# Kernel optimization log

Measured on AMD Instinct MI355X. Metric: run time of the kernel, lower is better.

The kernel has to match this reference:

```python
import jax, jax.numpy as jnp
import numpy as np

N_HEAD = 16
N_KV_HEAD = 4
D_HEAD = 128
RMS_EPS = 1.1920929e-07  # torch default eps for fp32 rms_norm


def _rms_norm(x):
    return x * jax.lax.rsqrt(jnp.mean(x * x, axis=-1, keepdims=True) + RMS_EPS)


def _rotary_tables(n_pos, dim):
    # dim = d_head; freq table has dim//2 entries (half of them zero)
    angular_freq = (1.0 / 1024.0) ** jnp.linspace(0.0, 1.0, dim // 4, dtype=jnp.float32)
    angular_freq = jnp.concatenate([angular_freq, jnp.zeros(dim // 4, jnp.float32)])
    theta = jnp.arange(n_pos, dtype=jnp.float32)[:, None] * angular_freq[None, :]
    return jnp.cos(theta), jnp.sin(theta)


def _apply_rotary(x):
    # x: (B, H, T, D). Faithful to source: cos/sin indexed by x.shape[-3] (= H),
    # broadcast over the time axis.
    n = x.shape[-3]
    cos, sin = _rotary_tables(n, x.shape[-1])
    cos = cos[None, :, None, :]
    sin = sin[None, :, None, :]
    xf = x.astype(jnp.float32)
    x1, x2 = jnp.split(xf, 2, axis=-1)
    y1 = x1 * cos + x2 * sin
    y2 = -x1 * sin + x2 * cos
    return jnp.concatenate([y1, y2], axis=-1).astype(x.dtype)


def setup_inputs() -> dict:
    key = jax.random.key(0)
    k1, k2, k3, k4 = jax.random.split(key, 4)
    B, T, C = 2, 2048, 2048
    return {
        "x": jax.random.normal(k1, (B, T, C), jnp.float32),
        "Wq": jax.random.normal(k2, (C, C), jnp.float32) * 0.02,
        "Wkv": jax.random.normal(k3, (2 * N_KV_HEAD * D_HEAD, C), jnp.float32) * 0.02,
        "Wproj": jax.random.normal(k4, (C, C), jnp.float32) * 0.02,
        "tok_masks": jnp.ones((B, T), jnp.int32),
    }


def reference(x, Wq, Wkv, Wproj, tok_masks):
    B, T, C = x.shape
    nh, nkv, dh = N_HEAD, N_KV_HEAD, D_HEAD

    q = (x @ Wq.T).reshape(B, T, nh, dh).transpose(0, 2, 1, 3)          # (B,nh,T,dh)
    kv = x @ Wkv.T                                                       # (B,T,2*nkv*dh)
    k, v = jnp.split(kv, 2, axis=2)
    k = k.reshape(B, T, nkv, dh).transpose(0, 2, 1, 3)                   # (B,nkv,T,dh)
    v = v.reshape(B, T, nkv, dh).transpose(0, 2, 1, 3)

    q, k = _rms_norm(q), _rms_norm(k)
    q, k = _apply_rotary(q), _apply_rotary(k)

    # GQA: repeat kv heads to match query heads
    rep = nh // nkv
    k = jnp.repeat(k, rep, axis=1)
    v = jnp.repeat(v, rep, axis=1)

    scale = 1.0 / jnp.sqrt(jnp.float32(dh))
    scores = jnp.einsum("bhqd,bhkd->bhqk", q, k) * scale                 # (B,nh,T,T)
    causal = jnp.tril(jnp.ones((T, T), bool))
    scores = jnp.where(causal[None, None], scores, -jnp.inf)
    attn = jax.nn.softmax(scores, axis=-1)
    y = jnp.einsum("bhqk,bhkd->bhqd", attn, v)                           # (B,nh,T,dh)
    y = y.transpose(0, 2, 1, 3).reshape(B, T, C)
    y = y @ Wproj.T
    return (y, jnp.float32(0.0))
```

## Files before the change

kernel.cpp:

```cpp
#include <hip/hip_runtime.h>
#include <hip/hip_bf16.h>

#define T_SEQ 2048
#define BATCH 2
#define CDIM  2048
#define NH    16
#define NKV   4
#define DH    128

typedef __attribute__((ext_vector_type(8))) short bfrag;
typedef __attribute__((ext_vector_type(4))) float ffrag;
typedef __hip_bfloat16 bf16;

#if defined(__has_builtin)
#if __has_builtin(__builtin_amdgcn_global_load_lds)
#define USE_GLL 1
#endif
#endif
#ifndef USE_GLL
#define USE_GLL 0
#endif

__device__ __forceinline__ void stage16(const bf16* __restrict__ g, bf16* lds_base, int lane) {
#if USE_GLL
    __builtin_amdgcn_global_load_lds((const __attribute__((address_space(1))) void*)g,
                                     (__attribute__((address_space(3))) void*)lds_base, 16, 0, 0);
#else
    *(bfrag*)(lds_base + lane * 8) = *(const bfrag*)g;
#endif
}

struct bf16x4 { bf16 a, b, c, d; };
#define N4_X   (BATCH * T_SEQ * CDIM / 4)
#define N4_WQ  (CDIM * CDIM / 4)
#define N4_WKV (2 * NKV * DH * CDIM / 4)
#define N4_WP  (CDIM * CDIM / 4)
__global__ __launch_bounds__(256) void cast_all(
    const float* __restrict__ x, const float* __restrict__ wq,
    const float* __restrict__ wkv, const float* __restrict__ wp,
    bf16* __restrict__ xb, bf16* __restrict__ wqb, bf16* __restrict__ wkvb, bf16* __restrict__ wpb)
{
    int j = blockIdx.x * 256 + threadIdx.x;
    const float* s; bf16* d;
    if (j < N4_X) { s = x; d = xb; }
    else {
        j -= N4_X;
        if (j < N4_WQ) { s = wq; d = wqb; }
        else {
            j -= N4_WQ;
            if (j < N4_WKV) { s = wkv; d = wkvb; }
            else { j -= N4_WKV; if (j >= N4_WP) return; s = wp; d = wpb; }
        }
    }
    float4 f = ((const float4*)s)[j];
    bf16x4 o{__float2bfloat16(f.x), __float2bfloat16(f.y),
             __float2bfloat16(f.z), __float2bfloat16(f.w)};
    ((bf16x4*)d)[j] = o;
}

template<int MODE>
__device__ __forceinline__ void gemm_body(
    const bf16* __restrict__ A, const bf16* __restrict__ W, int m0, int n0,
    bf16* __restrict__ out0, bf16* __restrict__ out1, float* __restrict__ outf)
{
    __shared__ __align__(16) bf16 sA[128 * 32];
    __shared__ __align__(16) bf16 sB[128 * 32];
    const int lane = threadIdx.x & 63;
    const int w = threadIdx.x >> 6;
    const int lr = lane & 15, quad = lane >> 4, lk = quad * 8;
    const int m_off = (w & 1) * 64, n_off = (w >> 1) * 64;

    const bf16* ap = A + (size_t)(m0 + w * 32 + (lane >> 2)) * CDIM + (lane & 3) * 8;
    const bf16* bp = W + (size_t)(n0 + w * 32 + (lane >> 2)) * CDIM + (lane & 3) * 8;
    bf16* sA0 = &sA[(w * 32) * 32];
    bf16* sA1 = &sA[(w * 32 + 16) * 32];
    bf16* sB0 = &sB[(w * 32) * 32];
    bf16* sB1 = &sB[(w * 32 + 16) * 32];

    ffrag acc[4][4] = {};
    for (int kk = 0; kk < CDIM; kk += 32) {
        __syncthreads();
        stage16(ap, sA0, lane);
        stage16(ap + (size_t)16 * CDIM, sA1, lane);
        stage16(bp, sB0, lane);
        stage16(bp + (size_t)16 * CDIM, sB1, lane);
        ap += 32; bp += 32;
        __syncthreads();

        bfrag af[4], bg[4];
        #pragma unroll
        for (int s = 0; s < 4; ++s) af[s] = *(const bfrag*)&sA[(m_off + s * 16 + lr) * 32 + lk];
        #pragma unroll
        for (int s = 0; s < 4; ++s) bg[s] = *(const bfrag*)&sB[(n_off + s * 16 + lr) * 32 + lk];
        #pragma unroll
        for (int i = 0; i < 4; ++i)
            #pragma unroll
            for (int j = 0; j < 4; ++j)
                acc[i][j] = __builtin_amdgcn_mfma_f32_16x16x32_bf16(af[i], bg[j], acc[i][j], 0, 0, 0);
    }

    #pragma unroll
    for (int si = 0; si < 4; ++si) {
        #pragma unroll
        for (int sj = 0; sj < 4; ++sj) {
            #pragma unroll
            for (int i = 0; i < 4; ++i) {
                int m = m0 + m_off + si * 16 + quad * 4 + i;
                int n = n0 + n_off + sj * 16 + lr;
                float v = acc[si][sj][i];
                if (MODE == 0) {
                    int b = m >> 11, t = m & (T_SEQ - 1);
                    int h = n >> 7, d = n & (DH - 1);
                    out0[(((size_t)(b * NH + h) * T_SEQ + t) << 7) + d] = __float2bfloat16(v);
                } else if (MODE == 1) {
                    int b = m >> 11, t = m & (T_SEQ - 1);
                    if (n < NKV * DH) {
                        int h = n >> 7, d = n & (DH - 1);
                        out0[(((size_t)(b * NKV + h) * T_SEQ + t) << 7) + d] = __float2bfloat16(v);
                    } else {
                        int n2 = n - NKV * DH;
                        int h = n2 >> 7, d = n2 & (DH - 1);
                        out1[(((size_t)(b * NKV + h) * DH + d) << 11) + t] = __float2bfloat16(v);
                    }
                } else {
                    outf[(size_t)m * CDIM + n] = v;
                }
            }
        }
    }
}

__global__ __launch_bounds__(256) void gemm_qkv(
    const bf16* __restrict__ A, const bf16* __restrict__ Wq, const bf16* __restrict__ Wkv,
    bf16* __restrict__ q, bf16* __restrict__ k, bf16* __restrict__ vt)
{
    if (blockIdx.y < 16)
        gemm_body<0>(A, Wq, blockIdx.x * 128, blockIdx.y * 128, q, nullptr, nullptr);
    else
        gemm_body<1>(A, Wkv, blockIdx.x * 128, (blockIdx.y - 16) * 128, k, vt, nullptr);
}

__global__ __launch_bounds__(256) void gemm_proj(
    const bf16* __restrict__ A, const bf16* __restrict__ W, float* __restrict__ outf)
{
    gemm_body<2>(A, W, blockIdx.x * 128, blockIdx.y * 128, nullptr, nullptr, outf);
    if (blockIdx.x == 0 && blockIdx.y == 0 && threadIdx.x == 0)
        outf[(size_t)BATCH * T_SEQ * CDIM] = 0.0f;
}

__global__ __launch_bounds__(256) void normrope_k(bf16* __restrict__ buf, int nheads) {
    const int row = blockIdx.x * 4 + (threadIdx.x >> 6);
    const int h = (row >> 11) % nheads;
    bf16* p = buf + (size_t)row * DH;
    const int d = threadIdx.x & 63;
    float x1 = __bfloat162float(p[d]);
    float x2 = __bfloat162float(p[d + 64]);
    float ss = x1 * x1 + x2 * x2;
    #pragma unroll
    for (int off = 32; off; off >>= 1) ss += __shfl_xor(ss, off);
    float r = rsqrtf(ss * (1.0f / 128.0f) + 1.1920929e-07f);
    x1 *= r; x2 *= r;
    float freq = (d < 32) ? exp2f(-10.0f * (float)d * (1.0f / 31.0f)) : 0.0f;
    float th = (float)h * freq;
    float c, s;
    __sincosf(th, &s, &c);
    p[d]      = __float2bfloat16(x1 * c + x2 * s);
    p[d + 64] = __float2bfloat16(-x1 * s + x2 * c);
}

#define PSTR 72
#define KSTR 136
#define VSTR 72
__global__ __launch_bounds__(256) void attn_k(const bf16* __restrict__ Q, const bf16* __restrict__ K,
                                              const bf16* __restrict__ VT, bf16* __restrict__ Y)
{
    const int lane = threadIdx.x & 63;
    const int w = threadIdx.x >> 6;
    const int p = blockIdx.x, h = blockIdx.y, b = blockIdx.z;
    const int lr = lane & 15, quad = lane >> 4, lk = quad * 8;
    const bf16* Qb = Q  + (size_t)(b * NH  + h)        * T_SEQ * DH;
    const bf16* Kb = K  + (size_t)(b * NKV + (h >> 2)) * T_SEQ * DH;
    const bf16* Vb = VT + (size_t)(b * NKV + (h >> 2)) * DH * T_SEQ;

    __shared__ __align__(16) bf16 SK[64 * KSTR];
    __shared__ __align__(16) bf16 SV[128 * VSTR];
    __shared__ __align__(16) bf16 SP[4][2][16 * PSTR];

    const int krow = w * 16 + (lane >> 4);
    const int kcol = (lane & 15) * 8;
    const int vrow = w * 32 + (lane >> 3);
    const int vcol = (lane & 7) * 8;
    const int prow = ((lr & 3) << 2) | (lr >> 2);
    const float scale = 0.08838834764831845f;

    for (int pass = 0; pass < 2; ++pass) {
        const int qb = pass ? (15 - p) : p;
        const int nc = 2 * (qb + 1);
        const int q0 = qb * 128 + w * 32;

        bfrag qf[2][4];
        #pragma unroll
        for (int t = 0; t < 2; ++t)
            #pragma unroll
            for (int dc = 0; dc < 4; ++dc)
                qf[t][dc] = *(const bfrag*)(Qb + (size_t)(q0 + t * 16 + lr) * DH + dc * 32 + lk);

        float lp[2][4] = {};
        ffrag o[2][8] = {};

        bfrag kr[4], vr[4];
        #pragma unroll
        for (int j = 0; j < 4; ++j) {
            kr[j] = *(const bfrag*)(Kb + (size_t)(krow + j * 4) * DH + kcol);
            vr[j] = *(const bfrag*)(Vb + (size_t)(vrow + j * 8) * T_SEQ + vcol);
        }

        for (int c = 0; c < nc; ++c) {
            const int base = c * 64;
            __syncthreads();
            #pragma unroll
            for (int j = 0; j < 4; ++j) {
                *(bfrag*)&SK[(size_t)(krow + j * 4) * KSTR + kcol] = kr[j];
                *(bfrag*)&SV[(size_t)(vrow + j * 8) * VSTR + vcol] = vr[j];
            }
            if (c + 1 < nc) {
                const int nb = base + 64;
                #pragma unroll
                for (int j = 0; j < 4; ++j) {
                    kr[j] = *(const bfrag*)(Kb + (size_t)(nb + krow + j * 4) * DH + kcol);
                    vr[j] = *(const bfrag*)(Vb + (size_t)(vrow + j * 8) * T_SEQ + nb + vcol);
                }
            }
            __syncthreads();

            ffrag s[2][4] = {};
            #pragma unroll
            for (int kt = 0; kt < 4; ++kt) {
                const bf16* kp = &SK[(kt * 16 + lr) * KSTR + lk];
                #pragma unroll
                for (int dc = 0; dc < 4; ++dc) {
                    bfrag kf = *(const bfrag*)(kp + dc * 32);
                    s[0][kt] = __builtin_amdgcn_mfma_f32_16x16x32_bf16(qf[0][dc], kf, s[0][kt], 0, 0, 0);
                    s[1][kt] = __builtin_amdgcn_mfma_f32_16x16x32_bf16(qf[1][dc], kf, s[1][kt], 0, 0, 0);
                }
            }

            const bool maskc = (c >= 2 * qb);
            #pragma unroll
            for (int t = 0; t < 2; ++t) {
                bf16* Pl = SP[w][t];
                #pragma unroll
                for (int kt = 0; kt < 4; ++kt) {
                    const int col = base + kt * 16 + lr;
                    #pragma unroll
                    for (int i = 0; i < 4; ++i) {
                        const int row = q0 + t * 16 + quad * 4 + i;
                        float e = (!maskc || col <= row) ? __expf(fmaf(s[t][kt][i], scale, -16.0f)) : 0.0f;
                        lp[t][i] += e;
                        Pl[(i * 4 + quad) * PSTR + kt * 16 + lr] = __float2bfloat16(e);
                    }
                }
            }

            bfrag pf[2][2];
            #pragma unroll
            for (int t = 0; t < 2; ++t) {
                pf[t][0] = *(const bfrag*)&SP[w][t][prow * PSTR + lk];
                pf[t][1] = *(const bfrag*)&SP[w][t][prow * PSTR + 32 + lk];
            }
            #pragma unroll
            for (int dt = 0; dt < 8; ++dt) {
                const bf16* vp = &SV[(dt * 16 + lr) * VSTR + lk];
                bfrag vf0 = *(const bfrag*)vp;
                bfrag vf1 = *(const bfrag*)(vp + 32);
                #pragma unroll
                for (int t = 0; t < 2; ++t) {
                    o[t][dt] = __builtin_amdgcn_mfma_f32_16x16x32_bf16(pf[t][0], vf0, o[t][dt], 0, 0, 0);
                    o[t][dt] = __builtin_amdgcn_mfma_f32_16x16x32_bf16(pf[t][1], vf1, o[t][dt], 0, 0, 0);
                }
            }
        }

        #pragma unroll
        for (int t = 0; t < 2; ++t) {
            float inv[4];
            #pragma unroll
            for (int i = 0; i < 4; ++i) {
                float l = lp[t][i];
                #pragma unroll
                for (int off = 1; off < 16; off <<= 1) l += __shfl_xor(l, off);
                inv[i] = 1.0f / l;
            }
            #pragma unroll
            for (int dt = 0; dt < 8; ++dt)
                #pragma unroll
                for (int i = 0; i < 4; ++i) {
                    int row = q0 + t * 16 + quad * 4 + i;
                    Y[((size_t)(b * T_SEQ) + row) * CDIM + h * DH + dt * 16 + lr] =
                        __float2bfloat16(o[t][dt][i] * inv[i]);
                }
        }
    }
}

extern "C" void kernel_launch(void* const* d_in, const int* in_sizes, int n_in,
                              void* d_out, int out_size, void* d_ws, size_t ws_size,
                              hipStream_t stream) {
    const float* x     = (const float*)d_in[0];
    const float* Wq    = (const float*)d_in[1];
    const float* Wkv   = (const float*)d_in[2];
    const float* Wproj = (const float*)d_in[3];
    float* out = (float*)d_out;

    char* ws = (char*)d_ws;
    size_t off = 0;
    auto alloc = [&](size_t bytes) { void* p = ws + off; off += (bytes + 255) & ~255ULL; return p; };
    bf16* xb   = (bf16*)alloc((size_t)BATCH * T_SEQ * CDIM * 2);
    bf16* wqb  = (bf16*)alloc((size_t)CDIM * CDIM * 2);
    bf16* wkvb = (bf16*)alloc((size_t)2 * NKV * DH * CDIM * 2);
    bf16* wpb  = (bf16*)alloc((size_t)CDIM * CDIM * 2);
    bf16* qb   = (bf16*)alloc((size_t)BATCH * NH * T_SEQ * DH * 2);
    bf16* kb   = (bf16*)alloc((size_t)BATCH * NKV * T_SEQ * DH * 2);
    bf16* vtb  = (bf16*)alloc((size_t)BATCH * NKV * DH * T_SEQ * 2);
    bf16* y1   = (bf16*)alloc((size_t)BATCH * T_SEQ * CDIM * 2);

    const int total4 = N4_X + N4_WQ + N4_WKV + N4_WP;
    cast_all<<<(total4 + 255) / 256, 256, 0, stream>>>(x, Wq, Wkv, Wproj, xb, wqb, wkvb, wpb);

    gemm_qkv<<<dim3(32, 24), 256, 0, stream>>>(xb, wqb, wkvb, qb, kb, vtb);
    normrope_k<<<BATCH * NH * T_SEQ / 4,  256, 0, stream>>>(qb, NH);
    normrope_k<<<BATCH * NKV * T_SEQ / 4, 256, 0, stream>>>(kb, NKV);
    attn_k<<<dim3(8, NH, BATCH), 256, 0, stream>>>(qb, kb, vtb, y1);
    gemm_proj<<<dim3(32, 16), 256, 0, stream>>>(y1, wpb, out);
}
```

Before: 314.3 us.

## Split attention KV across two wave groups, swizzle LDS, merge norm-rope launches

The attention kernel now runs 512 threads split into two wave groups. Each group handles alternating 32-key halves of every 64-key chunk for the same query rows, and the partial outputs and row sums are merged through shared memory at the end. Padded LDS strides in the GEMM and attention kernels are replaced by XOR swizzles to avoid bank conflicts without padding. The two norm-rope launches are fused into one. This raises parallelism per block but adds a cross-group reduction and extra barriers.

Result: faster. 302.1 us (-3.9%).

```diff
diff --git a/kernel.cpp b/kernel.cpp
--- a/kernel.cpp
+++ b/kernel.cpp
@@ -67,15 +67,20 @@
     __shared__ __align__(16) bf16 sB[128 * 32];
     const int lane = threadIdx.x & 63;
     const int w = threadIdx.x >> 6;
-    const int lr = lane & 15, quad = lane >> 4, lk = quad * 8;
+    const int lr = lane & 15, quad = lane >> 4;
     const int m_off = (w & 1) * 64, n_off = (w >> 1) * 64;
 
-    const bf16* ap = A + (size_t)(m0 + w * 32 + (lane >> 2)) * CDIM + (lane & 3) * 8;
-    const bf16* bp = W + (size_t)(n0 + w * 32 + (lane >> 2)) * CDIM + (lane & 3) * 8;
+    const int srow = lane >> 2;
+    const int ssw  = (srow + (srow >> 2)) & 3;
+    const bf16* ap = A + (size_t)(m0 + w * 32 + srow) * CDIM + (((lane & 3) ^ ssw)) * 8;
+    const bf16* bp = W + (size_t)(n0 + w * 32 + srow) * CDIM + (((lane & 3) ^ ssw)) * 8;
     bf16* sA0 = &sA[(w * 32) * 32];
     bf16* sA1 = &sA[(w * 32 + 16) * 32];
     bf16* sB0 = &sB[(w * 32) * 32];
     bf16* sB1 = &sB[(w * 32 + 16) * 32];
+
+    const int rsw = (lr + (lr >> 2)) & 3;
+    const int ccol = ((quad ^ rsw)) * 8;
 
     ffrag acc[4][4] = {};
     for (int kk = 0; kk < CDIM; kk += 32) {
@@ -89,9 +94,9 @@
 
         bfrag af[4], bg[4];
         #pragma unroll
-        for (int s = 0; s < 4; ++s) af[s] = *(const bfrag*)&sA[(m_off + s * 16 + lr) * 32 + lk];
-        #pragma unroll
-        for (int s = 0; s < 4; ++s) bg[s] = *(const bfrag*)&sB[(n_off + s * 16 + lr) * 32 + lk];
+        for (int s = 0; s < 4; ++s) af[s] = *(const bfrag*)&sA[(m_off + s * 16 + lr) * 32 + ccol];
+        #pragma unroll
+        for (int s = 0; s < 4; ++s) bg[s] = *(const bfrag*)&sB[(n_off + s * 16 + lr) * 32 + ccol];
         #pragma unroll
         for (int i = 0; i < 4; ++i)
             #pragma unroll
@@ -148,10 +153,15 @@
         outf[(size_t)BATCH * T_SEQ * CDIM] = 0.0f;
 }
 
-__global__ __launch_bounds__(256) void normrope_k(bf16* __restrict__ buf, int nheads) {
-    const int row = blockIdx.x * 4 + (threadIdx.x >> 6);
+#define QROWS (BATCH * NH * T_SEQ)
+#define KROWS (BATCH * NKV * T_SEQ)
+__global__ __launch_bounds__(256) void normrope_k(bf16* __restrict__ qb, bf16* __restrict__ kb) {
+    int row = blockIdx.x * 4 + (threadIdx.x >> 6);
+    bf16* bufb; int nheads;
+    if (row < QROWS) { bufb = qb; nheads = NH; }
+    else { row -= QROWS; bufb = kb; nheads = NKV; }
     const int h = (row >> 11) % nheads;
-    bf16* p = buf + (size_t)row * DH;
+    bf16* p = bufb + (size_t)row * DH;
     const int d = threadIdx.x & 63;
     float x1 = __bfloat162float(p[d]);
     float x2 = __bfloat162float(p[d + 64]);
@@ -168,35 +178,38 @@
     p[d + 64] = __float2bfloat16(-x1 * s + x2 * c);
 }
 
-#define PSTR 72
-#define KSTR 136
-#define VSTR 72
-__global__ __launch_bounds__(256) void attn_k(const bf16* __restrict__ Q, const bf16* __restrict__ K,
-                                              const bf16* __restrict__ VT, bf16* __restrict__ Y)
+__global__ __launch_bounds__(512, 2) void attn_k(const bf16* __restrict__ Q, const bf16* __restrict__ K,
+                                                 const bf16* __restrict__ VT, bf16* __restrict__ Y)
 {
     const int lane = threadIdx.x & 63;
     const int w = threadIdx.x >> 6;
+    const int g = w >> 2, wl = w & 3;
     const int p = blockIdx.x, h = blockIdx.y, b = blockIdx.z;
     const int lr = lane & 15, quad = lane >> 4, lk = quad * 8;
     const bf16* Qb = Q  + (size_t)(b * NH  + h)        * T_SEQ * DH;
     const bf16* Kb = K  + (size_t)(b * NKV + (h >> 2)) * T_SEQ * DH;
     const bf16* Vb = VT + (size_t)(b * NKV + (h >> 2)) * DH * T_SEQ;
 
-    __shared__ __align__(16) bf16 SK[64 * KSTR];
-    __shared__ __align__(16) bf16 SV[128 * VSTR];
-    __shared__ __align__(16) bf16 SP[4][2][16 * PSTR];
-
-    const int krow = w * 16 + (lane >> 4);
-    const int kcol = (lane & 15) * 8;
-    const int vrow = w * 32 + (lane >> 3);
-    const int vcol = (lane & 7) * 8;
-    const int prow = ((lr & 3) << 2) | (lr >> 2);
+    __shared__ __align__(16) union ShmU {
+        struct { bf16 SK[2][32 * 128]; bf16 SV[2][128 * 32]; bf16 SP[8][2][16 * 32]; } s;
+        ffrag MRG[9 * 4 * 64];
+    } shm;
+    bf16* SKg = shm.s.SK[g];
+    bf16* SVg = shm.s.SV[g];
+
+    const int k_r0 = wl * 8 + (lane >> 4);
+    const int k_ch = lane & 15;
+    const int v_r0 = wl * 32 + (lane >> 2);
+    const int v_ch = lane & 3;
+    const int vsw = (lr + (lr >> 2)) & 3;
+    const int prow_r = ((lr & 3) << 2) | (lr >> 2);
+    const int psw = (prow_r + (prow_r >> 2)) & 3;
     const float scale = 0.08838834764831845f;
 
     for (int pass = 0; pass < 2; ++pass) {
         const int qb = pass ? (15 - p) : p;
         const int nc = 2 * (qb + 1);
-        const int q0 = qb * 128 + w * 32;
+        const int q0 = qb * 128 + wl * 32;
 
         bfrag qf[2][4];
         #pragma unroll
@@ -208,97 +221,105 @@
         float lp[2][4] = {};
         ffrag o[2][8] = {};
 
-        bfrag kr[4], vr[4];
-        #pragma unroll
-        for (int j = 0; j < 4; ++j) {
-            kr[j] = *(const bfrag*)(Kb + (size_t)(krow + j * 4) * DH + kcol);
-            vr[j] = *(const bfrag*)(Vb + (size_t)(vrow + j * 8) * T_SEQ + vcol);
+        bfrag kr[2], vr[2];
+        {
+            const int b0 = g * 32;
+            #pragma unroll
+            for (int j = 0; j < 2; ++j) {
+                kr[j] = *(const bfrag*)(Kb + (size_t)(b0 + k_r0 + j * 4) * DH + k_ch * 8);
+                vr[j] = *(const bfrag*)(Vb + (size_t)(v_r0 + j * 16) * T_SEQ + b0 + v_ch * 8);
+            }
         }
 
         for (int c = 0; c < nc; ++c) {
-            const int base = c * 64;
+            const int base = c * 64 + g * 32;
             __syncthreads();
             #pragma unroll
-            for (int j = 0; j < 4; ++j) {
-                *(bfrag*)&SK[(size_t)(krow + j * 4) * KSTR + kcol] = kr[j];
-                *(bfrag*)&SV[(size_t)(vrow + j * 8) * VSTR + vcol] = vr[j];
+            for (int j = 0; j < 2; ++j) {
+                int krow = k_r0 + j * 4;
+                *(bfrag*)&SKg[krow * 128 + ((k_ch ^ (krow & 15))) * 8] = kr[j];
+                int vrow = v_r0 + j * 16;
+                *(bfrag*)&SVg[vrow * 32 + ((v_ch ^ ((vrow + (vrow >> 2)) & 3))) * 8] = vr[j];
             }
             if (c + 1 < nc) {
                 const int nb = base + 64;
                 #pragma unroll
-                for (int j = 0; j < 4; ++j) {
-                    kr[j] = *(const bfrag*)(Kb + (size_t)(nb + krow + j * 4) * DH + kcol);
-                    vr[j] = *(const bfrag*)(Vb + (size_t)(vrow + j * 8) * T_SEQ + nb + vcol);
+                for (int j = 0; j < 2; ++j) {
+                    kr[j] = *(const bfrag*)(Kb + (size_t)(nb + k_r0 + j * 4) * DH + k_ch * 8);
+                    vr[j] = *(const bfrag*)(Vb + (size_t)(v_r0 + j * 16) * T_SEQ + nb + v_ch * 8);
                 }
             }
             __syncthreads();
 
-            ffrag s[2][4] = {};
-            #pragma unroll
-            for (int kt = 0; kt < 4; ++kt) {
-                const bf16* kp = &SK[(kt * 16 + lr) * KSTR + lk];
+            ffrag s2[2][2] = {};
+            #pragma unroll
+            for (int kt = 0; kt < 2; ++kt)
                 #pragma unroll
                 for (int dc = 0; dc < 4; ++dc) {
-                    bfrag kf = *(const bfrag*)(kp + dc * 32);
-                    s[0][kt] = __builtin_amdgcn_mfma_f32_16x16x32_bf16(qf[0][dc], kf, s[0][kt], 0, 0, 0);
-                    s[1][kt] = __builtin_amdgcn_mfma_f32_16x16x32_bf16(qf[1][dc], kf, s[1][kt], 0, 0, 0);
-                }
-            }
+                    bfrag kf = *(const bfrag*)&SKg[(kt * 16 + lr) * 128 + (((dc << 2) | quad) ^ lr) * 8];
+                    s2[0][kt] = __builtin_amdgcn_mfma_f32_16x16x32_bf16(qf[0][dc], kf, s2[0][kt], 0, 0, 0);
+                    s2[1][kt] = __builtin_amdgcn_mfma_f32_16x16x32_bf16(qf[1][dc], kf, s2[1][kt], 0, 0, 0);
+                }
 
             const bool maskc = (c >= 2 * qb);
             #pragma unroll
-            for (int t = 0; t < 2; ++t) {
-                bf16* Pl = SP[w][t];
-                #pragma unroll
-                for (int kt = 0; kt < 4; ++kt) {
+            for (int t = 0; t < 2; ++t)
+                #pragma unroll
+                for (int kt = 0; kt < 2; ++kt) {
                     const int col = base + kt * 16 + lr;
                     #pragma unroll
                     for (int i = 0; i < 4; ++i) {
                         const int row = q0 + t * 16 + quad * 4 + i;
-                        float e = (!maskc || col <= row) ? __expf(fmaf(s[t][kt][i], scale, -16.0f)) : 0.0f;
+                        float e = (!maskc || col <= row) ? __expf(fmaf(s2[t][kt][i], scale, -16.0f)) : 0.0f;
                         lp[t][i] += e;
-                        Pl[(i * 4 + quad) * PSTR + kt * 16 + lr] = __float2bfloat16(e);
+                        const int pr = i * 4 + quad;
+                        const int pc = (kt * 2 + (lr >> 3)) ^ ((quad + i) & 3);
+                        shm.s.SP[w][t][pr * 32 + pc * 8 + (lr & 7)] = __float2bfloat16(e);
                     }
                 }
-            }
-
-            bfrag pf[2][2];
-            #pragma unroll
-            for (int t = 0; t < 2; ++t) {
-                pf[t][0] = *(const bfrag*)&SP[w][t][prow * PSTR + lk];
-                pf[t][1] = *(const bfrag*)&SP[w][t][prow * PSTR + 32 + lk];
-            }
+
+            bfrag pf0 = *(const bfrag*)&shm.s.SP[w][0][prow_r * 32 + ((quad ^ psw)) * 8];
+            bfrag pf1 = *(const bfrag*)&shm.s.SP[w][1][prow_r * 32 + ((quad ^ psw)) * 8];
             #pragma unroll
             for (int dt = 0; dt < 8; ++dt) {
-                const bf16* vp = &SV[(dt * 16 + lr) * VSTR + lk];
-                bfrag vf0 = *(const bfrag*)vp;
-                bfrag vf1 = *(const bfrag*)(vp + 32);
-                #pragma unroll
-                for (int t = 0; t < 2; ++t) {
-                    o[t][dt] = __builtin_amdgcn_mfma_f32_16x16x32_bf16(pf[t][0], vf0, o[t][dt], 0, 0, 0);
-                    o[t][dt] = __builtin_amdgcn_mfma_f32_16x16x32_bf16(pf[t][1], vf1, o[t][dt], 0, 0, 0);
-                }
-            }
-        }
-
+                bfrag vf = *(const bfrag*)&SVg[(dt * 16 + lr) * 32 + ((quad ^ vsw)) * 8];
+                o[0][dt] = __builtin_amdgcn_mfma_f32_16x16x32_bf16(pf0, vf, o[0][dt], 0, 0, 0);
+                o[1][dt] = __builtin_amdgcn_mfma_f32_16x16x32_bf16(pf1, vf, o[1][dt], 0, 0, 0);
+            }
+        }
+
+        __syncthreads();
         #pragma unroll
         for (int t = 0; t < 2; ++t) {
-            float inv[4];
-            #pragma unroll
-            for (int i = 0; i < 4; ++i) {
-                float l = lp[t][i];
-                #pragma unroll
-                for (int off = 1; off < 16; off <<= 1) l += __shfl_xor(l, off);
-                inv[i] = 1.0f / l;
-            }
-            #pragma unroll
-            for (int dt = 0; dt < 8; ++dt)
+            if (g == 1) {
+                #pragma unroll
+                for (int d = 0; d < 8; ++d) shm.MRG[(d * 4 + wl) * 64 + lane] = o[t][d];
+                ffrag l4 = {lp[t][0], lp[t][1], lp[t][2], lp[t][3]};
+                shm.MRG[(8 * 4 + wl) * 64 + lane] = l4;
+            }
+            __syncthreads();
+            if (g == 0) {
+                #pragma unroll
+                for (int d = 0; d < 8; ++d) o[t][d] += shm.MRG[(d * 4 + wl) * 64 + lane];
+                ffrag l4 = shm.MRG[(8 * 4 + wl) * 64 + lane];
+                float inv[4];
                 #pragma unroll
                 for (int i = 0; i < 4; ++i) {
-                    int row = q0 + t * 16 + quad * 4 + i;
-                    Y[((size_t)(b * T_SEQ) + row) * CDIM + h * DH + dt * 16 + lr] =
-                        __float2bfloat16(o[t][dt][i] * inv[i]);
-                }
+                    float l = lp[t][i] + l4[i];
+                    #pragma unroll
+                    for (int off = 1; off < 16; off <<= 1) l += __shfl_xor(l, off);
+                    inv[i] = 1.0f / l;
+                }
+                #pragma unroll
+                for (int dt = 0; dt < 8; ++dt)
+                    #pragma unroll
+                    for (int i = 0; i < 4; ++i) {
+                        int row = q0 + t * 16 + quad * 4 + i;
+                        Y[((size_t)(b * T_SEQ) + row) * CDIM + h * DH + dt * 16 + lr] =
+                            __float2bfloat16(o[t][dt][i] * inv[i]);
+                    }
+            }
+            __syncthreads();
         }
     }
 }
@@ -328,8 +349,7 @@
     cast_all<<<(total4 + 255) / 256, 256, 0, stream>>>(x, Wq, Wkv, Wproj, xb, wqb, wkvb, wpb);
 
     gemm_qkv<<<dim3(32, 24), 256, 0, stream>>>(xb, wqb, wkvb, qb, kb, vtb);
-    normrope_k<<<BATCH * NH * T_SEQ / 4,  256, 0, stream>>>(qb, NH);
-    normrope_k<<<BATCH * NKV * T_SEQ / 4, 256, 0, stream>>>(kb, NKV);
-    attn_k<<<dim3(8, NH, BATCH), 256, 0, stream>>>(qb, kb, vtb, y1);
+    normrope_k<<<(QROWS + KROWS) / 4, 256, 0, stream>>>(qb, kb);
+    attn_k<<<dim3(8, NH, BATCH), 512, 0, stream>>>(qb, kb, vtb, y1);
     gemm_proj<<<dim3(32, 16), 256, 0, stream>>>(y1, wpb, out);
 }
```
